# Kernel optimization log

Hardware: AMD Instinct MI355X
Metric: run time of the kernel (lower is better)

## Reference

```python
import jax, jax.numpy as jnp
import numpy as np

N_NODES = 50000
N_EDGES = 800000
D = 64
H = 4
EPS = 1e-5  # BatchNorm1d default eps


def setup_inputs() -> dict:
    key = jax.random.key(0)
    k1, k2, k3, k4, k5 = jax.random.split(key, 5)
    return {
        "h": jax.random.normal(k1, (N_NODES, D), dtype=jnp.float32),
        "e": jax.random.normal(k2, (N_EDGES, D), dtype=jnp.float32),
        "norm": jax.random.uniform(k3, (N_NODES, 1), dtype=jnp.float32),
        "gamma": jnp.ones((H, D), dtype=jnp.float32),
        "beta": jnp.zeros((H, D), dtype=jnp.float32),
        "src": jax.random.randint(k4, (N_EDGES,), 0, N_NODES, dtype=jnp.int32),
        "dst": jax.random.randint(k5, (N_EDGES,), 0, N_NODES, dtype=jnp.int32),
    }


def _segment_softmax(scores, seg, n):
    # numerically-stable softmax over incoming edges of each dst node
    m = jax.ops.segment_max(scores, seg, num_segments=n)
    m = jnp.where(jnp.isfinite(m), m, 0.0)  # empty segments -> 0
    ex = jnp.exp(scores - m[seg])
    denom = jax.ops.segment_sum(ex, seg, num_segments=n)
    return ex / denom[seg]


def reference(h, e, norm, gamma, beta, src, dst):
    z = h * norm  # [N, D]
    # edge attention score: dot(z_src, z_dst), then attn activation (relu)
    z_src = z[src]  # [E, D]
    scores = jax.nn.relu(jnp.sum(z_src * z[dst], axis=-1))  # [E]
    # segment softmax over mailbox (incoming edges per dst node)
    alpha = _segment_softmax(scores, dst, N_NODES)  # [E]
    # weighted scatter-sum aggregation (identical across heads: no per-head proj)
    agg = jax.ops.segment_sum(alpha[:, None] * z_src, dst, num_segments=N_NODES)  # [N, D]
    # BatchNorm1d in training mode (biased variance), per-head affine
    mean = jnp.mean(agg, axis=0)
    var = jnp.var(agg, axis=0)
    xhat = (agg - mean) / jnp.sqrt(var + EPS)  # [N, D]
    # per-head: gamma*xhat + beta -> relu -> * norm ; then concat over heads
    heads = jax.nn.relu(gamma[:, None, :] * xhat[None] + beta[:, None, :]) * norm[None]  # [H, N, D]
    h_out = jnp.transpose(heads, (1, 0, 2)).reshape(N_NODES, H * D)
    return h_out, e
```

## Files before the change

kernel.cpp:

```cpp
#include <hip/hip_runtime.h>
#include <hip/hip_bf16.h>

#define BLK 256
static constexpr float EPS = 1e-5f;
static constexpr int CAP = 64;

typedef float f32x4 __attribute__((ext_vector_type(4)));

__device__ inline unsigned short f2bf(float f) {
  unsigned int u = __float_as_uint(f);
  return (unsigned short)((u + 0x7fffu + ((u >> 16) & 1u)) >> 16);
}
__device__ inline unsigned int pack2(float lo, float hi) {
  return (unsigned int)f2bf(lo) | ((unsigned int)f2bf(hi) << 16);
}
__device__ inline float blo(unsigned int u) { return __uint_as_float(u << 16); }
__device__ inline float bhi(unsigned int u) { return __uint_as_float(u & 0xffff0000u); }

__device__ inline void do_copy(const f32x4* __restrict__ s, f32x4* __restrict__ d,
                               int lo, int hi, int tid, int nthr) {
  int i = lo + tid;
  for (; i + 3 * nthr < hi; i += 4 * nthr) {
    f32x4 v0 = __builtin_nontemporal_load(&s[i]);
    f32x4 v1 = __builtin_nontemporal_load(&s[i + nthr]);
    f32x4 v2 = __builtin_nontemporal_load(&s[i + 2 * nthr]);
    f32x4 v3 = __builtin_nontemporal_load(&s[i + 3 * nthr]);
    __builtin_nontemporal_store(v0, &d[i]);
    __builtin_nontemporal_store(v1, &d[i + nthr]);
    __builtin_nontemporal_store(v2, &d[i + 2 * nthr]);
    __builtin_nontemporal_store(v3, &d[i + 3 * nthr]);
  }
  for (; i < hi; i += nthr) {
    f32x4 v = __builtin_nontemporal_load(&s[i]);
    __builtin_nontemporal_store(v, &d[i]);
  }
}

__global__ void k_prep(const float* __restrict__ hbuf, const float* __restrict__ norm,
                       uint4* __restrict__ z, int n8, int* __restrict__ cursor,
                       float* __restrict__ sums, int nNodes,
                       const f32x4* __restrict__ esrc, f32x4* __restrict__ edst,
                       int cLo, int cHi, int ncopy) {
  int b = blockIdx.x;
  if (b < ncopy) {
    do_copy(esrc, edst, cLo, cHi, b * BLK + (int)threadIdx.x, ncopy * BLK);
    return;
  }
  int i = (b - ncopy) * BLK + threadIdx.x;
  if (i < nNodes) cursor[i] = 0;
  if (i < 128) sums[i] = 0.f;
  if (i >= n8) return;
  float s = norm[i >> 3];
  const float4* hp = reinterpret_cast<const float4*>(hbuf) + (size_t)i * 2;
  float4 a = hp[0], bb = hp[1];
  uint4 o;
  o.x = pack2(a.x * s, a.y * s);
  o.y = pack2(a.z * s, a.w * s);
  o.z = pack2(bb.x * s, bb.y * s);
  o.w = pack2(bb.z * s, bb.w * s);
  z[i] = o;
}

__global__ void k_scat(const int* __restrict__ src, const int* __restrict__ dst,
                       int* __restrict__ cursor, int* __restrict__ csr, int nE,
                       const f32x4* __restrict__ esrc, f32x4* __restrict__ edst,
                       int cLo, int cHi, int ncopy) {
  int b = blockIdx.x;
  if (b < ncopy) {
    do_copy(esrc, edst, cLo, cHi, b * BLK + (int)threadIdx.x, ncopy * BLK);
    return;
  }
  int e = (b - ncopy) * BLK + threadIdx.x;
  if (e >= nE) return;
  int d = dst[e];
  int slot = atomicAdd(&cursor[d], 1);
  if (slot < CAP) csr[d * CAP + slot] = src[e];
}

#define EDGE(r, vv)                                                            \
  {                                                                            \
    float a0 = blo(r.x), a1 = bhi(r.x), a2 = blo(r.y), a3 = bhi(r.y);          \
    float a4 = blo(r.z), a5 = bhi(r.z), a6 = blo(r.w), a7 = bhi(r.w);          \
    float p = a0 * d0;                                                         \
    p = fmaf(a1, d1, p); p = fmaf(a2, d2, p); p = fmaf(a3, d3, p);             \
    p = fmaf(a4, d4, p); p = fmaf(a5, d5, p); p = fmaf(a6, d6, p);             \
    p = fmaf(a7, d7, p);                                                       \
    p += __shfl_xor(p, 1);                                                     \
    p += __shfl_xor(p, 2);                                                     \
    p += __shfl_xor(p, 4);                                                     \
    p = fmaxf(p, 0.f);                                                         \
    float wv = (vv) ? __expf(p - 64.f) : 0.f;                                  \
    dsum += wv;                                                                \
    acc0 = fmaf(wv, a0, acc0); acc1 = fmaf(wv, a1, acc1);                      \
    acc2 = fmaf(wv, a2, acc2); acc3 = fmaf(wv, a3, acc3);                      \
    acc4 = fmaf(wv, a4, acc4); acc5 = fmaf(wv, a5, acc5);                      \
    acc6 = fmaf(wv, a6, acc6); acc7 = fmaf(wv, a7, acc7);                      \
  }

__global__ void k_fused(const uint4* __restrict__ z4, const int* __restrict__ cursor,
                        const int* __restrict__ csr, float4* __restrict__ agg4, int n,
                        const f32x4* __restrict__ esrc, f32x4* __restrict__ edst,
                        int cLo, int cHi, int ncopy) {
  int b = blockIdx.x;
  if (b < ncopy) {
    do_copy(esrc, edst, cLo, cHi, b * BLK + (int)threadIdx.x, ncopy * BLK);
    return;
  }
  int w = (b - ncopy) * (BLK / 64) + ((int)threadIdx.x >> 6);
  if (w >= n) return;
  int lane = threadIdx.x & 63;
  int sub = lane & 7, grp = lane >> 3;
  int cnt = min(cursor[w], CAP);
  int beg = w * CAP;

  int myIdx = (lane < cnt) ? csr[beg + lane] : 0;

  uint4 zd = z4[(size_t)w * 8 + sub];
  float d0 = blo(zd.x), d1 = bhi(zd.x), d2 = blo(zd.y), d3 = bhi(zd.y);
  float d4 = blo(zd.z), d5 = bhi(zd.z), d6 = blo(zd.w), d7 = bhi(zd.w);

  float dsum = 0.f;
  float acc0 = 0.f, acc1 = 0.f, acc2 = 0.f, acc3 = 0.f;
  float acc4 = 0.f, acc5 = 0.f, acc6 = 0.f, acc7 = 0.f;

  for (int base = 0; base < cnt; base += 32) {
    int j0 = base + grp, j1 = j0 + 8, j2 = j0 + 16, j3 = j0 + 24;
    bool v0 = j0 < cnt, v1 = j1 < cnt, v2 = j2 < cnt, v3 = j3 < cnt;
    int s0 = __shfl(myIdx, j0), s1 = __shfl(myIdx, j1);
    int s2 = __shfl(myIdx, j2), s3 = __shfl(myIdx, j3);
    uint4 r0 = z4[(size_t)(v0 ? s0 : 0) * 8 + sub];
    uint4 r1 = z4[(size_t)(v1 ? s1 : 0) * 8 + sub];
    uint4 r2 = z4[(size_t)(v2 ? s2 : 0) * 8 + sub];
    uint4 r3 = z4[(size_t)(v3 ? s3 : 0) * 8 + sub];
    EDGE(r0, v0)
    EDGE(r1, v1)
    EDGE(r2, v2)
    EDGE(r3, v3)
  }
  #pragma unroll
  for (int off = 8; off < 64; off <<= 1) {
    dsum += __shfl_xor(dsum, off);
    acc0 += __shfl_xor(acc0, off); acc1 += __shfl_xor(acc1, off);
    acc2 += __shfl_xor(acc2, off); acc3 += __shfl_xor(acc3, off);
    acc4 += __shfl_xor(acc4, off); acc5 += __shfl_xor(acc5, off);
    acc6 += __shfl_xor(acc6, off); acc7 += __shfl_xor(acc7, off);
  }
  float inv = (dsum > 0.f) ? 1.0f / dsum : 0.f;
  if (grp == 0) {
    agg4[(size_t)w * 16 + sub * 2 + 0] =
        make_float4(acc0 * inv, acc1 * inv, acc2 * inv, acc3 * inv);
    agg4[(size_t)w * 16 + sub * 2 + 1] =
        make_float4(acc4 * inv, acc5 * inv, acc6 * inv, acc7 * inv);
  }
}

__global__ void k_stats(const float* __restrict__ agg, float* __restrict__ sums, int n) {
  __shared__ float ls[128];
  if (threadIdx.x < 128) ls[threadIdx.x] = 0.f;
  __syncthreads();
  int col = threadIdx.x & 63;
  int rq  = threadIdx.x >> 6;
  int rend = min(n, (int)(blockIdx.x + 1) * 256);
  float s = 0.f, s2 = 0.f;
  for (int r = blockIdx.x * 256 + rq; r < rend; r += 4) {
    float v = agg[(size_t)r * 64 + col];
    s += v; s2 += v * v;
  }
  atomicAdd(&ls[col], s);
  atomicAdd(&ls[64 + col], s2);
  __syncthreads();
  if (threadIdx.x < 128) unsafeAtomicAdd(&sums[threadIdx.x], ls[threadIdx.x]);
}

__global__ void k_out(const float* __restrict__ agg, const float* __restrict__ sums,
                      const float* __restrict__ gamma, const float* __restrict__ beta,
                      const float* __restrict__ norm, f32x4* __restrict__ out, int n64,
                      float invN) {
  __shared__ float4 sm4[16], si4[16];
  float* sm = (float*)sm4;
  float* si = (float*)si4;
  if (threadIdx.x < 64) {
    float mu = sums[threadIdx.x] * invN;
    sm[threadIdx.x] = mu;
    si[threadIdx.x] = rsqrtf(sums[64 + threadIdx.x] * invN - mu * mu + EPS);
  }
  __syncthreads();
  int g = blockIdx.x * BLK + threadIdx.x;
  if (g >= n64) return;
  int node = g >> 6, within = g & 63;
  int head = within >> 4, d4 = within & 15;
  float4 a  = reinterpret_cast<const float4*>(agg)[(size_t)node * 16 + d4];
  float4 mu = sm4[d4];
  float4 iv = si4[d4];
  float4 ga = reinterpret_cast<const float4*>(gamma)[head * 16 + d4];
  float4 be = reinterpret_cast<const float4*>(beta)[head * 16 + d4];
  float s = norm[node];
  f32x4 r;
  r.x = fmaxf(fmaf(ga.x, (a.x - mu.x) * iv.x, be.x), 0.f) * s;
  r.y = fmaxf(fmaf(ga.y, (a.y - mu.y) * iv.y, be.y), 0.f) * s;
  r.z = fmaxf(fmaf(ga.z, (a.z - mu.z) * iv.z, be.z), 0.f) * s;
  r.w = fmaxf(fmaf(ga.w, (a.w - mu.w) * iv.w, be.w), 0.f) * s;
  __builtin_nontemporal_store(r, &out[g]);
}

__global__ void k_tail(const f32x4* __restrict__ esrc, f32x4* __restrict__ edst, int n4) {
  do_copy(esrc, edst, 0, n4, blockIdx.x * BLK + (int)threadIdx.x, gridDim.x * BLK);
}

extern "C" void kernel_launch(void* const* d_in, const int* in_sizes, int n_in,
                              void* d_out, int out_size, void* d_ws, size_t ws_size,
                              hipStream_t stream) {
  const float* h     = (const float*)d_in[0];
  const float* e     = (const float*)d_in[1];
  const float* norm  = (const float*)d_in[2];
  const float* gamma = (const float*)d_in[3];
  const float* beta  = (const float*)d_in[4];
  const int*   src   = (const int*)d_in[5];
  const int*   dst   = (const int*)d_in[6];
  const int N = in_sizes[2];
  const int E = in_sizes[5];
  float* out = (float*)d_out;

  float* eout = out + (size_t)N * 256;
  size_t eBytes = (size_t)E * 64 * sizeof(float);

  size_t need = 0;
  auto sz = [&](size_t b) { size_t o = need; need += (b + 255) & ~(size_t)255; return o; };
  size_t oZ    = sz((size_t)N * 64 * sizeof(unsigned short));
  size_t oAgg  = sz((size_t)N * 64 * sizeof(float));
  size_t oCsr  = sz((size_t)N * CAP * sizeof(int));
  size_t oCur  = sz((size_t)N * sizeof(int));
  size_t oSums = sz(128 * sizeof(float));

  bool useWs = (ws_size >= need);
  char* scratch = useWs ? (char*)d_ws : ((char*)eout + (eBytes - need));

  uint4* z      = (uint4*)(scratch + oZ);
  float* agg    = (float*)(scratch + oAgg);
  int*   csr    = (int*)  (scratch + oCsr);
  int*   cursor = (int*)  (scratch + oCur);
  float* sums   = (float*)(scratch + oSums);

  size_t headBytes = useWs ? eBytes : (eBytes - need);
  int headF4 = (int)(headBytes / 16);
  int tailF4 = (int)((eBytes - headBytes) / 16);

  int c1 = (int)((size_t)headF4 * 25 / 100) & ~15;
  int c2 = (int)((size_t)headF4 * 55 / 100) & ~15;

  const f32x4* e4  = (const f32x4*)e;
  f32x4*       eo4 = (f32x4*)eout;

  const int NC1 = 512, NC2 = 512, NC3 = 768;

  int n8 = N * 8;
  int zzB = (n8 + BLK - 1) / BLK;
  k_prep<<<NC1 + zzB, BLK, 0, stream>>>(h, norm, z, n8, cursor, sums, N,
                                        e4, eo4, 0, c1, NC1);

  int scB = (E + BLK - 1) / BLK;
  k_scat<<<NC2 + scB, BLK, 0, stream>>>(src, dst, cursor, csr, E,
                                        e4, eo4, c1, c2, NC2);

  int ndB = (N + 3) / 4;
  k_fused<<<NC3 + ndB, BLK, 0, stream>>>(z, cursor, csr, (float4*)agg, N,
                                         e4, eo4, c2, headF4, NC3);

  k_stats<<<(N + 255) / 256, 256, 0, stream>>>(agg, sums, N);

  int n64 = N * 64;
  k_out<<<(n64 + BLK - 1) / BLK, BLK, 0, stream>>>(agg, sums, gamma, beta, norm,
                                                   (f32x4*)out, n64, 1.0f / (float)N);

  if (tailF4 > 0)
    k_tail<<<1024, BLK, 0, stream>>>(e4 + headF4, eo4 + headF4, tailF4);
}
```

Baseline: 168.3 us.

## Fuse BatchNorm statistics into aggregation kernel and spread edge copy into output kernel

```diff
diff --git a/kernel.cpp b/kernel.cpp
--- a/kernel.cpp
+++ b/kernel.cpp
@@ -4,6 +4,7 @@
 #define BLK 256
 static constexpr float EPS = 1e-5f;
 static constexpr int CAP = 64;
+static constexpr int NPART = 64;
 
 typedef float f32x4 __attribute__((ext_vector_type(4)));
 
@@ -38,7 +39,7 @@
 
 __global__ void k_prep(const float* __restrict__ hbuf, const float* __restrict__ norm,
                        uint4* __restrict__ z, int n8, int* __restrict__ cursor,
-                       float* __restrict__ sums, int nNodes,
+                       float* __restrict__ partials, int nNodes,
                        const f32x4* __restrict__ esrc, f32x4* __restrict__ edst,
                        int cLo, int cHi, int ncopy) {
   int b = blockIdx.x;
@@ -48,7 +49,7 @@
   }
   int i = (b - ncopy) * BLK + threadIdx.x;
   if (i < nNodes) cursor[i] = 0;
-  if (i < 128) sums[i] = 0.f;
+  if (i < NPART * 128) partials[i] = 0.f;
   if (i >= n8) return;
   float s = norm[i >> 3];
   const float4* hp = reinterpret_cast<const float4*>(hbuf) + (size_t)i * 2;
@@ -98,7 +99,8 @@
   }
 
 __global__ void k_fused(const uint4* __restrict__ z4, const int* __restrict__ cursor,
-                        const int* __restrict__ csr, float4* __restrict__ agg4, int n,
+                        const int* __restrict__ csr, float4* __restrict__ agg4,
+                        float* __restrict__ partials, int n,
                         const f32x4* __restrict__ esrc, f32x4* __restrict__ edst,
                         int cLo, int cHi, int ncopy) {
   int b = blockIdx.x;
@@ -106,86 +108,104 @@
     do_copy(esrc, edst, cLo, cHi, b * BLK + (int)threadIdx.x, ncopy * BLK);
     return;
   }
-  int w = (b - ncopy) * (BLK / 64) + ((int)threadIdx.x >> 6);
-  if (w >= n) return;
+  __shared__ float shbuf[128];
+  if (threadIdx.x < 128) shbuf[threadIdx.x] = 0.f;
+  __syncthreads();
+
+  int cb = b - ncopy;
+  int w = cb * (BLK / 64) + ((int)threadIdx.x >> 6);
   int lane = threadIdx.x & 63;
   int sub = lane & 7, grp = lane >> 3;
-  int cnt = min(cursor[w], CAP);
-  int beg = w * CAP;
-
-  int myIdx = (lane < cnt) ? csr[beg + lane] : 0;
-
-  uint4 zd = z4[(size_t)w * 8 + sub];
-  float d0 = blo(zd.x), d1 = bhi(zd.x), d2 = blo(zd.y), d3 = bhi(zd.y);
-  float d4 = blo(zd.z), d5 = bhi(zd.z), d6 = blo(zd.w), d7 = bhi(zd.w);
-
-  float dsum = 0.f;
-  float acc0 = 0.f, acc1 = 0.f, acc2 = 0.f, acc3 = 0.f;
-  float acc4 = 0.f, acc5 = 0.f, acc6 = 0.f, acc7 = 0.f;
-
-  for (int base = 0; base < cnt; base += 32) {
-    int j0 = base + grp, j1 = j0 + 8, j2 = j0 + 16, j3 = j0 + 24;
-    bool v0 = j0 < cnt, v1 = j1 < cnt, v2 = j2 < cnt, v3 = j3 < cnt;
-    int s0 = __shfl(myIdx, j0), s1 = __shfl(myIdx, j1);
-    int s2 = __shfl(myIdx, j2), s3 = __shfl(myIdx, j3);
-    uint4 r0 = z4[(size_t)(v0 ? s0 : 0) * 8 + sub];
-    uint4 r1 = z4[(size_t)(v1 ? s1 : 0) * 8 + sub];
-    uint4 r2 = z4[(size_t)(v2 ? s2 : 0) * 8 + sub];
-    uint4 r3 = z4[(size_t)(v3 ? s3 : 0) * 8 + sub];
-    EDGE(r0, v0)
-    EDGE(r1, v1)
-    EDGE(r2, v2)
-    EDGE(r3, v3)
-  }
-  #pragma unroll
-  for (int off = 8; off < 64; off <<= 1) {
-    dsum += __shfl_xor(dsum, off);
-    acc0 += __shfl_xor(acc0, off); acc1 += __shfl_xor(acc1, off);
-    acc2 += __shfl_xor(acc2, off); acc3 += __shfl_xor(acc3, off);
-    acc4 += __shfl_xor(acc4, off); acc5 += __shfl_xor(acc5, off);
-    acc6 += __shfl_xor(acc6, off); acc7 += __shfl_xor(acc7, off);
-  }
-  float inv = (dsum > 0.f) ? 1.0f / dsum : 0.f;
-  if (grp == 0) {
-    agg4[(size_t)w * 16 + sub * 2 + 0] =
-        make_float4(acc0 * inv, acc1 * inv, acc2 * inv, acc3 * inv);
-    agg4[(size_t)w * 16 + sub * 2 + 1] =
-        make_float4(acc4 * inv, acc5 * inv, acc6 * inv, acc7 * inv);
-  }
-}
-
-__global__ void k_stats(const float* __restrict__ agg, float* __restrict__ sums, int n) {
+  if (w < n) {
+    int cnt = min(cursor[w], CAP);
+    int beg = w * CAP;
+    int myIdx = (lane < cnt) ? csr[beg + lane] : 0;
+
+    uint4 zd = z4[(size_t)w * 8 + sub];
+    float d0 = blo(zd.x), d1 = bhi(zd.x), d2 = blo(zd.y), d3 = bhi(zd.y);
+    float d4 = blo(zd.z), d5 = bhi(zd.z), d6 = blo(zd.w), d7 = bhi(zd.w);
+
+    float dsum = 0.f;
+    float acc0 = 0.f, acc1 = 0.f, acc2 = 0.f, acc3 = 0.f;
+    float acc4 = 0.f, acc5 = 0.f, acc6 = 0.f, acc7 = 0.f;
+
+    for (int base = 0; base < cnt; base += 32) {
+      int j0 = base + grp, j1 = j0 + 8, j2 = j0 + 16, j3 = j0 + 24;
+      bool v0 = j0 < cnt, v1 = j1 < cnt, v2 = j2 < cnt, v3 = j3 < cnt;
+      int s0 = __shfl(myIdx, j0), s1 = __shfl(myIdx, j1);
+      int s2 = __shfl(myIdx, j2), s3 = __shfl(myIdx, j3);
+      uint4 r0 = z4[(size_t)(v0 ? s0 : 0) * 8 + sub];
+      uint4 r1 = z4[(size_t)(v1 ? s1 : 0) * 8 + sub];
+      uint4 r2 = z4[(size_t)(v2 ? s2 : 0) * 8 + sub];
+      uint4 r3 = z4[(size_t)(v3 ? s3 : 0) * 8 + sub];
+      EDGE(r0, v0)
+      EDGE(r1, v1)
+      EDGE(r2, v2)
+      EDGE(r3, v3)
+    }
+    #pragma unroll
+    for (int off = 8; off < 64; off <<= 1) {
+      dsum += __shfl_xor(dsum, off);
+      acc0 += __shfl_xor(acc0, off); acc1 += __shfl_xor(acc1, off);
+      acc2 += __shfl_xor(acc2, off); acc3 += __shfl_xor(acc3, off);
+      acc4 += __shfl_xor(acc4, off); acc5 += __shfl_xor(acc5, off);
+      acc6 += __shfl_xor(acc6, off); acc7 += __shfl_xor(acc7, off);
+    }
+    float inv = (dsum > 0.f) ? 1.0f / dsum : 0.f;
+    if (grp == 0) {
+      float v0 = acc0 * inv, v1 = acc1 * inv, v2 = acc2 * inv, v3 = acc3 * inv;
+      float v4 = acc4 * inv, v5 = acc5 * inv, v6 = acc6 * inv, v7 = acc7 * inv;
+      agg4[(size_t)w * 16 + sub * 2 + 0] = make_float4(v0, v1, v2, v3);
+      agg4[(size_t)w * 16 + sub * 2 + 1] = make_float4(v4, v5, v6, v7);
+      int c = sub * 8;
+      atomicAdd(&shbuf[c + 0], v0); atomicAdd(&shbuf[64 + c + 0], v0 * v0);
+      atomicAdd(&shbuf[c + 1], v1); atomicAdd(&shbuf[64 + c + 1], v1 * v1);
+      atomicAdd(&shbuf[c + 2], v2); atomicAdd(&shbuf[64 + c + 2], v2 * v2);
+      atomicAdd(&shbuf[c + 3], v3); atomicAdd(&shbuf[64 + c + 3], v3 * v3);
+      atomicAdd(&shbuf[c + 4], v4); atomicAdd(&shbuf[64 + c + 4], v4 * v4);
+      atomicAdd(&shbuf[c + 5], v5); atomicAdd(&shbuf[64 + c + 5], v5 * v5);
+      atomicAdd(&shbuf[c + 6], v6); atomicAdd(&shbuf[64 + c + 6], v6 * v6);
+      atomicAdd(&shbuf[c + 7], v7); atomicAdd(&shbuf[64 + c + 7], v7 * v7);
+    }
+  }
+  __syncthreads();
+  if (threadIdx.x < 128)
+    unsafeAtomicAdd(&partials[(cb & (NPART - 1)) * 128 + threadIdx.x], shbuf[threadIdx.x]);
+}
+
+__global__ void k_finalize(const float* __restrict__ partials, float* __restrict__ stats,
+                           float invN) {
   __shared__ float ls[128];
-  if (threadIdx.x < 128) ls[threadIdx.x] = 0.f;
+  int t = threadIdx.x;
+  float s = 0.f;
+  for (int k = 0; k < NPART; ++k) s += partials[k * 128 + t];
+  ls[t] = s;
   __syncthreads();
-  int col = threadIdx.x & 63;
-  int rq  = threadIdx.x >> 6;
-  int rend = min(n, (int)(blockIdx.x + 1) * 256);
-  float s = 0.f, s2 = 0.f;
-  for (int r = blockIdx.x * 256 + rq; r < rend; r += 4) {
-    float v = agg[(size_t)r * 64 + col];
-    s += v; s2 += v * v;
-  }
-  atomicAdd(&ls[col], s);
-  atomicAdd(&ls[64 + col], s2);
-  __syncthreads();
-  if (threadIdx.x < 128) unsafeAtomicAdd(&sums[threadIdx.x], ls[threadIdx.x]);
-}
-
-__global__ void k_out(const float* __restrict__ agg, const float* __restrict__ sums,
+  if (t < 64) {
+    float mu = ls[t] * invN;
+    stats[t] = mu;
+    stats[64 + t] = rsqrtf(ls[64 + t] * invN - mu * mu + EPS);
+  }
+}
+
+__global__ void k_out(const float* __restrict__ agg, const float* __restrict__ stats,
                       const float* __restrict__ gamma, const float* __restrict__ beta,
                       const float* __restrict__ norm, f32x4* __restrict__ out, int n64,
-                      float invN) {
+                      const f32x4* __restrict__ esrc, f32x4* __restrict__ edst,
+                      int cLo, int cHi, int ncopy) {
+  int b = blockIdx.x;
+  if (b < ncopy) {
+    do_copy(esrc, edst, cLo, cHi, b * BLK + (int)threadIdx.x, ncopy * BLK);
+    return;
+  }
   __shared__ float4 sm4[16], si4[16];
-  float* sm = (float*)sm4;
-  float* si = (float*)si4;
-  if (threadIdx.x < 64) {
-    float mu = sums[threadIdx.x] * invN;
-    sm[threadIdx.x] = mu;
-    si[threadIdx.x] = rsqrtf(sums[64 + threadIdx.x] * invN - mu * mu + EPS);
+  if (threadIdx.x < 32) {
+    ((float4*)sm4)[threadIdx.x & 15] = ((const float4*)stats)[threadIdx.x & 15];
+    if (threadIdx.x >= 16)
+      ((float4*)si4)[threadIdx.x & 15] = ((const float4*)stats)[16 + (threadIdx.x & 15)];
   }
   __syncthreads();
-  int g = blockIdx.x * BLK + threadIdx.x;
+  int g = (b - ncopy) * BLK + threadIdx.x;
   if (g >= n64) return;
   int node = g >> 6, within = g & 63;
   int head = within >> 4, d4 = within & 15;
@@ -230,32 +250,35 @@
   size_t oAgg  = sz((size_t)N * 64 * sizeof(float));
   size_t oCsr  = sz((size_t)N * CAP * sizeof(int));
   size_t oCur  = sz((size_t)N * sizeof(int));
-  size_t oSums = sz(128 * sizeof(float));
+  size_t oPart = sz((size_t)NPART * 128 * sizeof(float));
+  size_t oStat = sz(128 * sizeof(float));
 
   bool useWs = (ws_size >= need);
   char* scratch = useWs ? (char*)d_ws : ((char*)eout + (eBytes - need));
 
-  uint4* z      = (uint4*)(scratch + oZ);
-  float* agg    = (float*)(scratch + oAgg);
-  int*   csr    = (int*)  (scratch + oCsr);
-  int*   cursor = (int*)  (scratch + oCur);
-  float* sums   = (float*)(scratch + oSums);
+  uint4* z        = (uint4*)(scratch + oZ);
+  float* agg      = (float*)(scratch + oAgg);
+  int*   csr      = (int*)  (scratch + oCsr);
+  int*   cursor   = (int*)  (scratch + oCur);
+  float* partials = (float*)(scratch + oPart);
+  float* stats    = (float*)(scratch + oStat);
 
   size_t headBytes = useWs ? eBytes : (eBytes - need);
   int headF4 = (int)(headBytes / 16);
   int tailF4 = (int)((eBytes - headBytes) / 16);
 
-  int c1 = (int)((size_t)headF4 * 25 / 100) & ~15;
-  int c2 = (int)((size_t)headF4 * 55 / 100) & ~15;
+  int c1 = (int)((size_t)headF4 * 22 / 100) & ~15;
+  int c2 = (int)((size_t)headF4 * 50 / 100) & ~15;
+  int c3 = (int)((size_t)headF4 * 85 / 100) & ~15;
 
   const f32x4* e4  = (const f32x4*)e;
   f32x4*       eo4 = (f32x4*)eout;
 
-  const int NC1 = 512, NC2 = 512, NC3 = 768;
+  const int NC1 = 512, NC2 = 512, NC3 = 768, NC4 = 384;
 
   int n8 = N * 8;
   int zzB = (n8 + BLK - 1) / BLK;
-  k_prep<<<NC1 + zzB, BLK, 0, stream>>>(h, norm, z, n8, cursor, sums, N,
+  k_prep<<<NC1 + zzB, BLK, 0, stream>>>(h, norm, z, n8, cursor, partials, N,
                                         e4, eo4, 0, c1, NC1);
 
   int scB = (E + BLK - 1) / BLK;
@@ -263,14 +286,15 @@
                                         e4, eo4, c1, c2, NC2);
 
   int ndB = (N + 3) / 4;
-  k_fused<<<NC3 + ndB, BLK, 0, stream>>>(z, cursor, csr, (float4*)agg, N,
-                                         e4, eo4, c2, headF4, NC3);
-
-  k_stats<<<(N + 255) / 256, 256, 0, stream>>>(agg, sums, N);
+  k_fused<<<NC3 + ndB, BLK, 0, stream>>>(z, cursor, csr, (float4*)agg, partials, N,
+                                         e4, eo4, c2, c3, NC3);
+
+  k_finalize<<<1, 128, 0, stream>>>(partials, stats, 1.0f / (float)N);
 
   int n64 = N * 64;
-  k_out<<<(n64 + BLK - 1) / BLK, BLK, 0, stream>>>(agg, sums, gamma, beta, norm,
-                                                   (f32x4*)out, n64, 1.0f / (float)N);
+  int outB = (n64 + BLK - 1) / BLK;
+  k_out<<<NC4 + outB, BLK, 0, stream>>>(agg, stats, gamma, beta, norm, (f32x4*)out,
+                                        n64, e4, eo4, c3, headF4, NC4);
 
   if (tailF4 > 0)
     k_tail<<<1024, BLK, 0, stream>>>(e4 + headF4, eo4 + headF4, tailF4);
```

Result: slower. 182.0 us (+8.1%).
